# Performance work log

Hardware: AMD Instinct MI355X
Metric: run time of the kernel (lower is better)

Reference implementation:

```python
import jax, jax.numpy as jnp
import numpy as np

B, S, D, H = 4, 8192, 1024, 16   # batch, seq, in_feature==out_feature, num_heads
SCALE = (D // H) ** -0.5          # torch: (key.size(-1) // num_heads) ** -0.5 = 64**-0.5
EPS = 1e-5


def setup_inputs() -> dict:
    key = jax.random.key(0)
    ks = jax.random.split(key, 8)
    return {
        "query": jax.random.normal(ks[0], (B, S, D), dtype=jnp.float32),
        "key": jax.random.normal(ks[1], (B, S, D), dtype=jnp.float32),
        "value": jax.random.normal(ks[2], (B, S, D), dtype=jnp.float32),
        "wq": jax.random.normal(ks[3], (D, D), dtype=jnp.float32) * 0.02,
        "wk": jax.random.normal(ks[4], (D, D), dtype=jnp.float32) * 0.02,
        "wv": jax.random.normal(ks[5], (D, D), dtype=jnp.float32) * 0.02,
        "w_final": jax.random.normal(ks[6], (D, D), dtype=jnp.float32) * 0.02,
        "b_final": jnp.zeros((D,), dtype=jnp.float32),
        "gamma": jnp.ones((D,), dtype=jnp.float32),
        "beta": jnp.zeros((D,), dtype=jnp.float32),
    }


def reference(query, key, value, wq, wk, wv, w_final, b_final, gamma, beta):
    residual = query
    # projections: [B, S, D]
    q = jnp.matmul(query, wq)
    k = jnp.matmul(key, wk)
    v = jnp.matmul(value, wv)
    # faithful to source: view splits the SEQUENCE dim into H blocks -> [B*H, S/H, D]
    q = q.reshape(B * H, S // H, D)
    k = k.reshape(B * H, S // H, D)
    v = v.reshape(B * H, S // H, D)
    # scaled dot-product attention per block (no mask, dropout=0)
    scores = jnp.einsum("bqd,bkd->bqk", q, k) * SCALE   # [B*H, S/H, S/H]
    attention = jax.nn.softmax(scores, axis=2)
    context = jnp.einsum("bqk,bkd->bqd", attention, v)   # [B*H, S/H, D]
    context = context.reshape(B, S, D)                   # dim_per_head*H == D
    output = jnp.matmul(context, w_final.T) + b_final
    # layernorm(residual + output)
    x = residual + output
    mean = jnp.mean(x, axis=-1, keepdims=True)
    var = jnp.var(x, axis=-1, keepdims=True)
    out = (x - mean) * jax.lax.rsqrt(var + EPS) * gamma + beta
    return (out, attention)
```

## Files before the change

### kernel.cpp

```cpp
#include <hip/hip_runtime.h>

typedef unsigned short u16;
typedef __bf16 bf16x8 __attribute__((ext_vector_type(8)));
typedef float floatx4 __attribute__((ext_vector_type(4)));


__device__ __forceinline__ u16 f2bf(float f) {
  union { float f; unsigned u; } x; x.f = f;
  unsigned r = x.u + 0x7FFFu + ((x.u >> 16) & 1u);
  return (u16)(r >> 16);
}

__device__ __forceinline__ void async16(const u16* g, u16* l) {
  __builtin_amdgcn_global_load_lds((const __attribute__((address_space(1))) void*)g,
                                   (__attribute__((address_space(3))) void*)l,
                                   16, 0, 0);
}

__global__ __launch_bounds__(256) void wconv_t(const float* __restrict__ wq,
                                               const float* __restrict__ wk,
                                               const float* __restrict__ wv,
                                               u16* __restrict__ dst0) {
  const float* src = blockIdx.z == 0 ? wq : (blockIdx.z == 1 ? wk : wv);
  u16* dst = dst0 + (size_t)blockIdx.z * 1024 * 1024;
  __shared__ float t[32][33];
  int k0 = blockIdx.y * 32, n0 = blockIdx.x * 32;
  int tid = threadIdx.x;
  int row = tid >> 3, c4 = (tid & 7) * 4;
  float4 v = *(const float4*)&src[(size_t)(k0 + row) * 1024 + n0 + c4];
  t[row][c4 + 0] = v.x; t[row][c4 + 1] = v.y; t[row][c4 + 2] = v.z; t[row][c4 + 3] = v.w;
  __syncthreads();
  ushort4 u;
  u.x = f2bf(t[c4 + 0][row]);
  u.y = f2bf(t[c4 + 1][row]);
  u.z = f2bf(t[c4 + 2][row]);
  u.w = f2bf(t[c4 + 3][row]);
  *(ushort4*)&dst[(size_t)(n0 + row) * 1024 + k0 + c4] = u;
}

__global__ __launch_bounds__(256) void wconv(const float* __restrict__ w, u16* __restrict__ dst) {
  size_t i = ((size_t)blockIdx.x * 256 + threadIdx.x) * 4;
  float4 v = *(const float4*)&w[i];
  ushort4 u; u.x = f2bf(v.x); u.y = f2bf(v.y); u.z = f2bf(v.z); u.w = f2bf(v.w);
  *(ushort4*)&dst[i] = u;
}

__global__ __launch_bounds__(256) void transpose_v(const u16* __restrict__ V,
                                                   u16* __restrict__ Vt) {
  __shared__ u16 t[64][65];
  const u16* src = V + (size_t)blockIdx.z * 512 * 1024;
  u16* dst = Vt + (size_t)blockIdx.z * 1024 * 512;
  int s0 = blockIdx.y * 64, d0 = blockIdx.x * 64;
  int tid = threadIdx.x;
#pragma unroll
  for (int i = 0; i < 4; ++i) {
    int row = i * 16 + (tid >> 4);
    int c4 = (tid & 15) * 4;
    ushort4 v = *(const ushort4*)&src[(size_t)(s0 + row) * 1024 + d0 + c4];
    t[row][c4 + 0] = v.x; t[row][c4 + 1] = v.y; t[row][c4 + 2] = v.z; t[row][c4 + 3] = v.w;
  }
  __syncthreads();
#pragma unroll
  for (int i = 0; i < 4; ++i) {
    int row = i * 16 + (tid >> 4);
    int c4 = (tid & 15) * 4;
    ushort4 u;
    u.x = t[c4 + 0][row]; u.y = t[c4 + 1][row]; u.z = t[c4 + 2][row]; u.w = t[c4 + 3][row];
    *(ushort4*)&dst[(size_t)(d0 + row) * 512 + s0 + c4] = u;
  }
}

template <int AF32, int OMODE>
__global__ __launch_bounds__(256) void gemm_bt(
    const void* __restrict__ Ap, const u16* __restrict__ Bp, void* __restrict__ Cp,
    int K, int lda, int ldb, int ldc,
    long long sA, long long sB, long long sC,
    const float* __restrict__ res, const float* __restrict__ bias, float scale) {
  __shared__ u16 Asm[128 * 32];
  __shared__ u16 Bsm[128 * 32];

  const int tid = threadIdx.x;
  const int wave = tid >> 6, lane = tid & 63;
  const int wm = wave >> 1, wn = wave & 1;
  const int quad = lane >> 4, r16 = lane & 15;
  const long long z = blockIdx.z;
  const size_t m0 = (size_t)blockIdx.y * 128;
  const size_t n0 = (size_t)blockIdx.x * 128;

  const u16* Bb = Bp + (size_t)(z * sB);
  floatx4 acc[4][4] = {};

  for (int k0 = 0; k0 < K; k0 += 32) {
    if constexpr (AF32) {
      const float* Af = (const float*)Ap + (size_t)(z * sA);
#pragma unroll
      for (int i = 0; i < 4; ++i) {
        int row = i * 32 + (tid >> 3);
        int col = (tid & 7) * 4;
        float4 v = *(const float4*)(Af + (m0 + row) * (size_t)lda + k0 + col);
        ushort4 u; u.x = f2bf(v.x); u.y = f2bf(v.y); u.z = f2bf(v.z); u.w = f2bf(v.w);
        *(ushort4*)&Asm[row * 32 + col] = u;
      }
    } else {
      const u16* Ab = (const u16*)Ap + (size_t)(z * sA);
#pragma unroll
      for (int c = 0; c < 2; ++c) {
        int chunk = c * 4 + wave;
        int row = chunk * 16 + (lane >> 2);
        int col = (lane & 3) * 8;
        async16(Ab + (m0 + row) * (size_t)lda + k0 + col, &Asm[chunk * 512]);
      }
    }
#pragma unroll
    for (int c = 0; c < 2; ++c) {
      int chunk = c * 4 + wave;
      int row = chunk * 16 + (lane >> 2);
      int col = (lane & 3) * 8;
      async16(Bb + (n0 + row) * (size_t)ldb + k0 + col, &Bsm[chunk * 512]);
    }
    __syncthreads();

    bf16x8 af[4], bfr[4];
#pragma unroll
    for (int i = 0; i < 4; ++i)
      af[i] = *(const bf16x8*)&Asm[(wm * 64 + i * 16 + r16) * 32 + quad * 8];
#pragma unroll
    for (int j = 0; j < 4; ++j)
      bfr[j] = *(const bf16x8*)&Bsm[(wn * 64 + j * 16 + r16) * 32 + quad * 8];
#pragma unroll
    for (int i = 0; i < 4; ++i)
#pragma unroll
      for (int j = 0; j < 4; ++j)
        acc[i][j] = __builtin_amdgcn_mfma_f32_16x16x32_bf16(af[i], bfr[j], acc[i][j], 0, 0, 0);
    __syncthreads();
  }

#pragma unroll
  for (int i = 0; i < 4; ++i) {
    size_t row = m0 + wm * 64 + i * 16 + quad * 4;
#pragma unroll
    for (int j = 0; j < 4; ++j) {
      size_t col = n0 + wn * 64 + j * 16 + r16;
#pragma unroll
      for (int r = 0; r < 4; ++r) {
        size_t idx = (row + r) * (size_t)ldc + col;
        if constexpr (OMODE == 0) {
          ((u16*)Cp)[(size_t)(z * sC) + idx] = f2bf(acc[i][j][r]);
        } else if constexpr (OMODE == 1) {
          ((float*)Cp)[(size_t)(z * sC) + idx] = acc[i][j][r] * scale;
        } else {
          float xv = acc[i][j][r] + bias[col] + res[idx];
          ((float*)Cp)[idx] = xv;
        }
      }
    }
  }
}

__global__ __launch_bounds__(256) void softmax_k(float* __restrict__ attn) {
  size_t row = (size_t)blockIdx.x * 4 + (threadIdx.x >> 6);
  int lane = threadIdx.x & 63;
  float* p = attn + row * 512 + lane * 8;
  float4 a = *(const float4*)p;
  float4 b = *(const float4*)(p + 4);
  float m = fmaxf(fmaxf(fmaxf(a.x, a.y), fmaxf(a.z, a.w)),
                  fmaxf(fmaxf(b.x, b.y), fmaxf(b.z, b.w)));
#pragma unroll
  for (int off = 32; off >= 1; off >>= 1) m = fmaxf(m, __shfl_xor(m, off));
  float e[8];
  e[0] = __expf(a.x - m); e[1] = __expf(a.y - m); e[2] = __expf(a.z - m); e[3] = __expf(a.w - m);
  e[4] = __expf(b.x - m); e[5] = __expf(b.y - m); e[6] = __expf(b.z - m); e[7] = __expf(b.w - m);
  float s = e[0] + e[1] + e[2] + e[3] + e[4] + e[5] + e[6] + e[7];
#pragma unroll
  for (int off = 32; off >= 1; off >>= 1) s += __shfl_xor(s, off);
  float inv = 1.0f / s;
  float4 oa, ob;
  oa.x = e[0] * inv; oa.y = e[1] * inv; oa.z = e[2] * inv; oa.w = e[3] * inv;
  ob.x = e[4] * inv; ob.y = e[5] * inv; ob.z = e[6] * inv; ob.w = e[7] * inv;
  *(float4*)p = oa;
  *(float4*)(p + 4) = ob;
}

__global__ __launch_bounds__(256) void layernorm_k(const float* __restrict__ x,
                                                   const float* __restrict__ gamma,
                                                   const float* __restrict__ beta,
                                                   float* __restrict__ out) {
  size_t row = blockIdx.x;
  int tid = threadIdx.x, lane = tid & 63, wave = tid >> 6;
  float4 v = *(const float4*)&x[row * 1024 + tid * 4];
  float s = v.x + v.y + v.z + v.w;
  float q = v.x * v.x + v.y * v.y + v.z * v.z + v.w * v.w;
#pragma unroll
  for (int off = 32; off >= 1; off >>= 1) {
    s += __shfl_xor(s, off);
    q += __shfl_xor(q, off);
  }
  __shared__ float ss[4], qq[4];
  if (lane == 0) { ss[wave] = s; qq[wave] = q; }
  __syncthreads();
  s = ss[0] + ss[1] + ss[2] + ss[3];
  q = qq[0] + qq[1] + qq[2] + qq[3];
  float mean = s * (1.0f / 1024.0f);
  float var = q * (1.0f / 1024.0f) - mean * mean;
  float rstd = rsqrtf(var + 1e-5f);
  float4 g = *(const float4*)&gamma[tid * 4];
  float4 be = *(const float4*)&beta[tid * 4];
  float4 o;
  o.x = (v.x - mean) * rstd * g.x + be.x;
  o.y = (v.y - mean) * rstd * g.y + be.y;
  o.z = (v.z - mean) * rstd * g.z + be.z;
  o.w = (v.w - mean) * rstd * g.w + be.w;
  *(float4*)&out[row * 1024 + tid * 4] = o;
}

extern "C" void kernel_launch(void* const* d_in, const int* in_sizes, int n_in,
                              void* d_out, int out_size, void* d_ws, size_t ws_size,
                              hipStream_t stream) {
  const float* query = (const float*)d_in[0];
  const float* key   = (const float*)d_in[1];
  const float* value = (const float*)d_in[2];
  const float* wq    = (const float*)d_in[3];
  const float* wk    = (const float*)d_in[4];
  const float* wv    = (const float*)d_in[5];
  const float* wfin  = (const float*)d_in[6];
  const float* bfin  = (const float*)d_in[7];
  const float* gamma = (const float*)d_in[8];
  const float* beta  = (const float*)d_in[9];

  char* ws = (char*)d_ws;
  u16* WQT = (u16*)(ws + 0);
  u16* WKT = WQT + 1024 * 1024;
  u16* WVT = WKT + 1024 * 1024;
  u16* WF  = WVT + 1024 * 1024;
  u16* Qb  = (u16*)(ws + 8388608);
  u16* Kb  = Qb + 33554432;
  u16* Vb  = Kb + 33554432;
  u16* VTb = Vb + 33554432;
  u16* CTX = VTb + 33554432;
  float* X = (float*)(ws + 8388608);

  float* out  = (float*)d_out;
  float* attn = out + 33554432;

  dim3 blk(256);

  wconv_t<<<dim3(32, 32, 3), blk, 0, stream>>>(wq, wk, wv, WQT);
  wconv<<<dim3(1024), blk, 0, stream>>>(wfin, WF);

  gemm_bt<1, 0><<<dim3(8, 256, 1), blk, 0, stream>>>(query, WQT, Qb, 1024, 1024, 1024, 1024,
                                                     0, 0, 0, nullptr, nullptr, 1.0f);
  gemm_bt<1, 0><<<dim3(8, 256, 1), blk, 0, stream>>>(key, WKT, Kb, 1024, 1024, 1024, 1024,
                                                     0, 0, 0, nullptr, nullptr, 1.0f);
  gemm_bt<1, 0><<<dim3(8, 256, 1), blk, 0, stream>>>(value, WVT, Vb, 1024, 1024, 1024, 1024,
                                                     0, 0, 0, nullptr, nullptr, 1.0f);

  transpose_v<<<dim3(16, 8, 64), blk, 0, stream>>>(Vb, VTb);

  gemm_bt<0, 1><<<dim3(4, 4, 64), blk, 0, stream>>>(Qb, Kb, attn, 1024, 1024, 1024, 512,
                                                    524288, 524288, 262144,
                                                    nullptr, nullptr, 0.125f);

  softmax_k<<<dim3(8192), blk, 0, stream>>>(attn);

  gemm_bt<1, 0><<<dim3(8, 4, 64), blk, 0, stream>>>(attn, VTb, CTX, 512, 512, 512, 1024,
                                                    262144, 524288, 524288,
                                                    nullptr, nullptr, 1.0f);

  gemm_bt<0, 2><<<dim3(8, 256, 1), blk, 0, stream>>>(CTX, WF, X, 1024, 1024, 1024, 1024,
                                                     0, 0, 0, query, bfin, 1.0f);

  layernorm_k<<<dim3(32768), blk, 0, stream>>>(X, gamma, beta, out);
}
```

Before: 1.249 ms.

## Pre-cast activations to bf16 and emit bf16 probabilities for async GEMM loads

Adds a separate cast kernel that converts query/key/value to bf16 once. The softmax also writes a bf16 copy of the probabilities, so every GEMM can use the async global-to-LDS path instead of in-loop fp32 loads and conversion. The fp32 A-operand path is removed, workspace buffers are reassigned to reuse memory, and single-batch GEMMs get a block-index swizzle meant to improve L2 locality. This costs an extra full read and write pass over the inputs and an extra bf16 probability buffer write.

After: 1.213 ms. 1.03x faster.

```diff
diff --git a/kernel.cpp b/kernel.cpp
--- a/kernel.cpp
+++ b/kernel.cpp
@@ -3,6 +3,7 @@
 typedef unsigned short u16;
 typedef __bf16 bf16x8 __attribute__((ext_vector_type(8)));
 typedef float floatx4 __attribute__((ext_vector_type(4)));
+typedef u16 u16x8 __attribute__((ext_vector_type(8)));
 
 
 __device__ __forceinline__ u16 f2bf(float f) {
@@ -45,6 +46,21 @@
   *(ushort4*)&dst[i] = u;
 }
 
+__global__ __launch_bounds__(256) void cast_bf16(const float* __restrict__ q,
+                                                 const float* __restrict__ k,
+                                                 const float* __restrict__ v,
+                                                 u16* __restrict__ dst0) {
+  const float* src = blockIdx.z == 0 ? q : (blockIdx.z == 1 ? k : v);
+  u16* dst = dst0 + (size_t)blockIdx.z * 33554432;
+  size_t i = ((size_t)blockIdx.x * 256 + threadIdx.x) * 8;
+  float4 a = *(const float4*)&src[i];
+  float4 b = *(const float4*)&src[i + 4];
+  u16x8 o;
+  o[0] = f2bf(a.x); o[1] = f2bf(a.y); o[2] = f2bf(a.z); o[3] = f2bf(a.w);
+  o[4] = f2bf(b.x); o[5] = f2bf(b.y); o[6] = f2bf(b.z); o[7] = f2bf(b.w);
+  *(u16x8*)&dst[i] = o;
+}
+
 __global__ __launch_bounds__(256) void transpose_v(const u16* __restrict__ V,
                                                    u16* __restrict__ Vt) {
   __shared__ u16 t[64][65];
@@ -70,9 +86,9 @@
   }
 }
 
-template <int AF32, int OMODE>
+template <int OMODE>
 __global__ __launch_bounds__(256) void gemm_bt(
-    const void* __restrict__ Ap, const u16* __restrict__ Bp, void* __restrict__ Cp,
+    const u16* __restrict__ Ap, const u16* __restrict__ Bp, void* __restrict__ Cp,
     int K, int lda, int ldb, int ldc,
     long long sA, long long sB, long long sC,
     const float* __restrict__ res, const float* __restrict__ bias, float scale) {
@@ -84,32 +100,31 @@
   const int wm = wave >> 1, wn = wave & 1;
   const int quad = lane >> 4, r16 = lane & 15;
   const long long z = blockIdx.z;
-  const size_t m0 = (size_t)blockIdx.y * 128;
-  const size_t n0 = (size_t)blockIdx.x * 128;
-
+
+  int bx = blockIdx.x, by = blockIdx.y;
+  if (gridDim.z == 1) {
+    unsigned nwg = gridDim.x * gridDim.y;
+    if ((nwg & 7u) == 0u) {
+      unsigned bid = (unsigned)by * gridDim.x + bx;
+      unsigned nb = (bid & 7u) * (nwg >> 3) + (bid >> 3);
+      bx = nb % gridDim.x;
+      by = nb / gridDim.x;
+    }
+  }
+  const size_t m0 = (size_t)by * 128;
+  const size_t n0 = (size_t)bx * 128;
+
+  const u16* Ab = Ap + (size_t)(z * sA);
   const u16* Bb = Bp + (size_t)(z * sB);
   floatx4 acc[4][4] = {};
 
   for (int k0 = 0; k0 < K; k0 += 32) {
-    if constexpr (AF32) {
-      const float* Af = (const float*)Ap + (size_t)(z * sA);
-#pragma unroll
-      for (int i = 0; i < 4; ++i) {
-        int row = i * 32 + (tid >> 3);
-        int col = (tid & 7) * 4;
-        float4 v = *(const float4*)(Af + (m0 + row) * (size_t)lda + k0 + col);
-        ushort4 u; u.x = f2bf(v.x); u.y = f2bf(v.y); u.z = f2bf(v.z); u.w = f2bf(v.w);
-        *(ushort4*)&Asm[row * 32 + col] = u;
-      }
-    } else {
-      const u16* Ab = (const u16*)Ap + (size_t)(z * sA);
-#pragma unroll
-      for (int c = 0; c < 2; ++c) {
-        int chunk = c * 4 + wave;
-        int row = chunk * 16 + (lane >> 2);
-        int col = (lane & 3) * 8;
-        async16(Ab + (m0 + row) * (size_t)lda + k0 + col, &Asm[chunk * 512]);
-      }
+#pragma unroll
+    for (int c = 0; c < 2; ++c) {
+      int chunk = c * 4 + wave;
+      int row = chunk * 16 + (lane >> 2);
+      int col = (lane & 3) * 8;
+      async16(Ab + (m0 + row) * (size_t)lda + k0 + col, &Asm[chunk * 512]);
     }
 #pragma unroll
     for (int c = 0; c < 2; ++c) {
@@ -157,7 +172,8 @@
   }
 }
 
-__global__ __launch_bounds__(256) void softmax_k(float* __restrict__ attn) {
+__global__ __launch_bounds__(256) void softmax_k(float* __restrict__ attn,
+                                                 u16* __restrict__ Pb) {
   size_t row = (size_t)blockIdx.x * 4 + (threadIdx.x >> 6);
   int lane = threadIdx.x & 63;
   float* p = attn + row * 512 + lane * 8;
@@ -174,11 +190,18 @@
 #pragma unroll
   for (int off = 32; off >= 1; off >>= 1) s += __shfl_xor(s, off);
   float inv = 1.0f / s;
+  float o[8];
+#pragma unroll
+  for (int i = 0; i < 8; ++i) o[i] = e[i] * inv;
   float4 oa, ob;
-  oa.x = e[0] * inv; oa.y = e[1] * inv; oa.z = e[2] * inv; oa.w = e[3] * inv;
-  ob.x = e[4] * inv; ob.y = e[5] * inv; ob.z = e[6] * inv; ob.w = e[7] * inv;
+  oa.x = o[0]; oa.y = o[1]; oa.z = o[2]; oa.w = o[3];
+  ob.x = o[4]; ob.y = o[5]; ob.z = o[6]; ob.w = o[7];
   *(float4*)p = oa;
   *(float4*)(p + 4) = ob;
+  u16x8 pb;
+#pragma unroll
+  for (int i = 0; i < 8; ++i) pb[i] = f2bf(o[i]);
+  *(u16x8*)&Pb[row * 512 + lane * 8] = pb;
 }
 
 __global__ __launch_bounds__(256) void layernorm_k(const float* __restrict__ x,
@@ -228,16 +251,20 @@
   const float* beta  = (const float*)d_in[9];
 
   char* ws = (char*)d_ws;
-  u16* WQT = (u16*)(ws + 0);
+  u16* WQT = (u16*)ws;
   u16* WKT = WQT + 1024 * 1024;
   u16* WVT = WKT + 1024 * 1024;
   u16* WF  = WVT + 1024 * 1024;
-  u16* Qb  = (u16*)(ws + 8388608);
+  u16* Qin = (u16*)(ws + 8388608);
+  u16* Kin = Qin + 33554432;
+  u16* Vin = Kin + 33554432;
+  u16* Qb  = (u16*)(ws + 209715200);
   u16* Kb  = Qb + 33554432;
-  u16* Vb  = Kb + 33554432;
-  u16* VTb = Vb + 33554432;
-  u16* CTX = VTb + 33554432;
-  float* X = (float*)(ws + 8388608);
+  u16* Vb  = Qin;
+  u16* VTb = Kin;
+  u16* Pb  = Vin;
+  u16* CTX = Qin;
+  float* X = (float*)(ws + 209715200);
 
   float* out  = (float*)d_out;
   float* attn = out + 33554432;
@@ -246,28 +273,29 @@
 
   wconv_t<<<dim3(32, 32, 3), blk, 0, stream>>>(wq, wk, wv, WQT);
   wconv<<<dim3(1024), blk, 0, stream>>>(wfin, WF);
-
-  gemm_bt<1, 0><<<dim3(8, 256, 1), blk, 0, stream>>>(query, WQT, Qb, 1024, 1024, 1024, 1024,
-                                                     0, 0, 0, nullptr, nullptr, 1.0f);
-  gemm_bt<1, 0><<<dim3(8, 256, 1), blk, 0, stream>>>(key, WKT, Kb, 1024, 1024, 1024, 1024,
-                                                     0, 0, 0, nullptr, nullptr, 1.0f);
-  gemm_bt<1, 0><<<dim3(8, 256, 1), blk, 0, stream>>>(value, WVT, Vb, 1024, 1024, 1024, 1024,
-                                                     0, 0, 0, nullptr, nullptr, 1.0f);
+  cast_bf16<<<dim3(16384, 1, 3), blk, 0, stream>>>(query, key, value, Qin);
+
+  gemm_bt<0><<<dim3(8, 256, 1), blk, 0, stream>>>(Qin, WQT, Qb, 1024, 1024, 1024, 1024,
+                                                  0, 0, 0, nullptr, nullptr, 1.0f);
+  gemm_bt<0><<<dim3(8, 256, 1), blk, 0, stream>>>(Kin, WKT, Kb, 1024, 1024, 1024, 1024,
+                                                  0, 0, 0, nullptr, nullptr, 1.0f);
+  gemm_bt<0><<<dim3(8, 256, 1), blk, 0, stream>>>(Vin, WVT, Vb, 1024, 1024, 1024, 1024,
+                                                  0, 0, 0, nullptr, nullptr, 1.0f);
 
   transpose_v<<<dim3(16, 8, 64), blk, 0, stream>>>(Vb, VTb);
 
-  gemm_bt<0, 1><<<dim3(4, 4, 64), blk, 0, stream>>>(Qb, Kb, attn, 1024, 1024, 1024, 512,
-                                                    524288, 524288, 262144,
-                                                    nullptr, nullptr, 0.125f);
-
-  softmax_k<<<dim3(8192), blk, 0, stream>>>(attn);
-
-  gemm_bt<1, 0><<<dim3(8, 4, 64), blk, 0, stream>>>(attn, VTb, CTX, 512, 512, 512, 1024,
-                                                    262144, 524288, 524288,
-                                                    nullptr, nullptr, 1.0f);
-
-  gemm_bt<0, 2><<<dim3(8, 256, 1), blk, 0, stream>>>(CTX, WF, X, 1024, 1024, 1024, 1024,
-                                                     0, 0, 0, query, bfin, 1.0f);
+  gemm_bt<1><<<dim3(4, 4, 64), blk, 0, stream>>>(Qb, Kb, attn, 1024, 1024, 1024, 512,
+                                                 524288, 524288, 262144,
+                                                 nullptr, nullptr, 0.125f);
+
+  softmax_k<<<dim3(8192), blk, 0, stream>>>(attn, Pb);
+
+  gemm_bt<0><<<dim3(8, 4, 64), blk, 0, stream>>>(Pb, VTb, CTX, 512, 512, 512, 1024,
+                                                 262144, 524288, 524288,
+                                                 nullptr, nullptr, 1.0f);
+
+  gemm_bt<2><<<dim3(8, 256, 1), blk, 0, stream>>>(CTX, WF, X, 1024, 1024, 1024, 1024,
+                                                  0, 0, 0, query, bfin, 1.0f);
 
   layernorm_k<<<dim3(32768), blk, 0, stream>>>(X, gamma, beta, out);
 }
```
